# Kernel optimization log

Measured on AMD Instinct MI355X. Metric: run time of the kernel, lower is better.

## Reference

```python
import jax, jax.numpy as jnp
import numpy as np

DENSE_SIZE = 2048
BATCH = 64
MAX_SPIKES = 1024


def setup_inputs() -> dict:
    key = jax.random.key(0)
    k_w, k_ids, k_ns = jax.random.split(key, 3)
    # weights ~ N(0, 2) as in tf.random_normal_initializer(0., 2., 42)
    W = jax.random.normal(k_w, (DENSE_SIZE, DENSE_SIZE), dtype=jnp.float32) * 2.0
    spike_ids = jax.random.randint(k_ids, (BATCH, MAX_SPIKES), 0, DENSE_SIZE, dtype=jnp.int32)
    num_spikes = jax.random.randint(k_ns, (BATCH,), 0, MAX_SPIKES, dtype=jnp.int32)
    return {"spike_ids": spike_ids, "num_spikes": num_spikes, "W": W}


def reference(spike_ids, num_spikes, W):
    # Dense-weight x binary-sparse-vector matmul:
    # out[b, j] = sum_{i < num_spikes[b]} W[j, spike_ids[b, i]]
    # i.e. gather active columns of W and sum them.
    mask = (jnp.arange(MAX_SPIKES)[None, :] < num_spikes[:, None]).astype(W.dtype)  # [B, S]
    cols = jnp.take(W.T, spike_ids, axis=0)  # [B, S, D] gathered columns (rows of W.T)
    out = jnp.einsum('bs,bsd->bd', mask, cols)  # [B, D]
    return out
```

## Files before the change

kernel.cpp:

```cpp
#include <hip/hip_runtime.h>

#define DENSE 2048
#define BATCH 64
#define MAXS  1024

typedef __attribute__((ext_vector_type(8))) __bf16 bf16x8;
typedef __attribute__((ext_vector_type(4))) float f32x4;


__global__ __launch_bounds__(256) void hist_kernel(const int* __restrict__ ids,
                                                   const int* __restrict__ ns,
                                                   __bf16* __restrict__ Cbf,
                                                   float* __restrict__ out) {
    __shared__ int cnt[DENSE];
    const int b = blockIdx.x;
    const int tid = threadIdx.x;
    #pragma unroll
    for (int k = tid; k < DENSE; k += 256) cnt[k] = 0;
    __syncthreads();
    const int n = ns[b];
    const int4 v = ((const int4*)(ids + b * MAXS))[tid];
    const int base = tid * 4;
    if (base + 0 < n) atomicAdd(&cnt[v.x], 1);
    if (base + 1 < n) atomicAdd(&cnt[v.y], 1);
    if (base + 2 < n) atomicAdd(&cnt[v.z], 1);
    if (base + 3 < n) atomicAdd(&cnt[v.w], 1);
    __syncthreads();
    const int mt = b >> 4;
    const int bl = b & 15;
    #pragma unroll
    for (int k = tid; k < DENSE; k += 256) {
        const int lane = bl | (((k >> 3) & 3) << 4);
        const size_t off = (size_t)(((k >> 5) * 4 + mt) * 64 + lane) * 8 + (k & 7);
        Cbf[off] = (__bf16)(float)cnt[k];
        out[(size_t)b * DENSE + k] = 0.0f;
    }
}

__global__ __launch_bounds__(256) void spmm_kernel(const float* __restrict__ W,
                                                   const __bf16* __restrict__ Cbf,
                                                   float* __restrict__ out) {
    const int tid  = threadIdx.x;
    const int lane = tid & 63;
    const int wv   = tid >> 6;
    const int j0   = blockIdx.x * 16;
    const int ks4  = blockIdx.y;

    const int ln = lane & 15;
    const int lq = lane >> 4;

    const int step0 = ks4 * 16 + wv * 4;
    const float* wrow = W + (size_t)(j0 + ln) * DENSE;

    f32x4 w0[4], w1[4];
    #pragma unroll
    for (int s = 0; s < 4; ++s) {
        const int kbase = (step0 + s) * 32 + lq * 8;
        w0[s] = *(const f32x4*)(wrow + kbase);
        w1[s] = *(const f32x4*)(wrow + kbase + 4);
    }
    bf16x8 afr[4][4];
    #pragma unroll
    for (int s = 0; s < 4; ++s) {
        #pragma unroll
        for (int mt = 0; mt < 4; ++mt) {
            afr[s][mt] = *(const bf16x8*)(Cbf + ((size_t)((step0 + s) * 4 + mt) * 64 + lane) * 8);
        }
    }

    bf16x8 wb[4];
    #pragma unroll
    for (int s = 0; s < 4; ++s) {
        #pragma unroll
        for (int i = 0; i < 4; ++i) {
            wb[s][i]     = (__bf16)w0[s][i];
            wb[s][i + 4] = (__bf16)w1[s][i];
        }
    }

    f32x4 acc[4];
    #pragma unroll
    for (int mt = 0; mt < 4; ++mt) acc[mt] = (f32x4)0.0f;
    #pragma unroll
    for (int s = 0; s < 4; ++s) {
        #pragma unroll
        for (int mt = 0; mt < 4; ++mt) {
            acc[mt] = __builtin_amdgcn_mfma_f32_16x16x32_bf16(afr[s][mt], wb[s], acc[mt], 0, 0, 0);
        }
    }

    __shared__ float P[4][4][4][64];
    #pragma unroll
    for (int mt = 0; mt < 4; ++mt) {
        #pragma unroll
        for (int r = 0; r < 4; ++r) {
            P[wv][mt][r][lane] = acc[mt][r];
        }
    }
    __syncthreads();

    const int jloc  = tid & 15;
    const int bpart = tid >> 4;
    const int lsrc  = ((bpart >> 2) << 4) | jloc;
    const int r     = bpart & 3;
    #pragma unroll
    for (int mt = 0; mt < 4; ++mt) {
        const float v = P[0][mt][r][lsrc] + P[1][mt][r][lsrc]
                      + P[2][mt][r][lsrc] + P[3][mt][r][lsrc];
        atomicAdd(&out[(size_t)(mt * 16 + bpart) * DENSE + j0 + jloc], v);
    }
}

extern "C" void kernel_launch(void* const* d_in, const int* in_sizes, int n_in,
                              void* d_out, int out_size, void* d_ws, size_t ws_size,
                              hipStream_t stream) {
    const int*   ids = (const int*)d_in[0];
    const int*   ns  = (const int*)d_in[1];
    const float* W   = (const float*)d_in[2];
    float*  out = (float*)d_out;
    __bf16* Cbf = (__bf16*)d_ws;

    hipLaunchKernelGGL(hist_kernel, dim3(BATCH), dim3(256), 0, stream, ids, ns, Cbf, out);
    hipLaunchKernelGGL(spmm_kernel, dim3(128, 4), dim3(256), 0, stream, W, Cbf, out);
}
```

Baseline: 72.28 us.

## Prefetch W into cache during histogram, drop K-split atomics, double-buffer spmm loads

After: 78.93 us. 1.09x slower.

```diff
diff --git a/kernel.cpp b/kernel.cpp
--- a/kernel.cpp
+++ b/kernel.cpp
@@ -10,82 +10,102 @@
 
 __global__ __launch_bounds__(256) void hist_kernel(const int* __restrict__ ids,
                                                    const int* __restrict__ ns,
+                                                   const float* __restrict__ W,
                                                    __bf16* __restrict__ Cbf,
-                                                   float* __restrict__ out) {
-    __shared__ int cnt[DENSE];
-    const int b = blockIdx.x;
+                                                   float* __restrict__ guard) {
     const int tid = threadIdx.x;
-    #pragma unroll
-    for (int k = tid; k < DENSE; k += 256) cnt[k] = 0;
-    __syncthreads();
-    const int n = ns[b];
-    const int4 v = ((const int4*)(ids + b * MAXS))[tid];
-    const int base = tid * 4;
-    if (base + 0 < n) atomicAdd(&cnt[v.x], 1);
-    if (base + 1 < n) atomicAdd(&cnt[v.y], 1);
-    if (base + 2 < n) atomicAdd(&cnt[v.z], 1);
-    if (base + 3 < n) atomicAdd(&cnt[v.w], 1);
-    __syncthreads();
-    const int mt = b >> 4;
-    const int bl = b & 15;
-    #pragma unroll
-    for (int k = tid; k < DENSE; k += 256) {
-        const int lane = bl | (((k >> 3) & 3) << 4);
-        const size_t off = (size_t)(((k >> 5) * 4 + mt) * 64 + lane) * 8 + (k & 7);
-        Cbf[off] = (__bf16)(float)cnt[k];
-        out[(size_t)b * DENSE + k] = 0.0f;
+    const int bid = blockIdx.x;
+    if (bid < BATCH) {
+        __shared__ int cnt[DENSE];
+        const int b = bid;
+        #pragma unroll
+        for (int k = tid; k < DENSE; k += 256) cnt[k] = 0;
+        __syncthreads();
+        const int n = ns[b];
+        const int4 v = ((const int4*)(ids + b * MAXS))[tid];
+        const int base = tid * 4;
+        if (base + 0 < n) atomicAdd(&cnt[v.x], 1);
+        if (base + 1 < n) atomicAdd(&cnt[v.y], 1);
+        if (base + 2 < n) atomicAdd(&cnt[v.z], 1);
+        if (base + 3 < n) atomicAdd(&cnt[v.w], 1);
+        __syncthreads();
+        const int mt = b >> 4;
+        const int bl = b & 15;
+        #pragma unroll
+        for (int k = tid; k < DENSE; k += 256) {
+            const int lane = bl | (((k >> 3) & 3) << 4);
+            const size_t off = (size_t)(((k >> 5) * 4 + mt) * 64 + lane) * 8 + (k & 7);
+            Cbf[off] = (__bf16)(float)cnt[k];
+        }
+    } else {
+        const int t = (bid - BATCH) * 256 + tid;
+        float s = 0.0f;
+        for (int i = t; i < (DENSE * DENSE) / 4; i += 192 * 256) {
+            const f32x4 v = ((const f32x4*)W)[i];
+            s += v.x + v.y + v.z + v.w;
+        }
+        if (s != s) guard[0] = s;
     }
 }
 
-__global__ __launch_bounds__(256) void spmm_kernel(const float* __restrict__ W,
-                                                   const __bf16* __restrict__ Cbf,
-                                                   float* __restrict__ out) {
+__global__ __launch_bounds__(256, 1) void spmm_kernel(const float* __restrict__ W,
+                                                      const __bf16* __restrict__ Cbf,
+                                                      float* __restrict__ out) {
     const int tid  = threadIdx.x;
     const int lane = tid & 63;
     const int wv   = tid >> 6;
     const int j0   = blockIdx.x * 16;
-    const int ks4  = blockIdx.y;
 
     const int ln = lane & 15;
     const int lq = lane >> 4;
 
-    const int step0 = ks4 * 16 + wv * 4;
     const float* wrow = W + (size_t)(j0 + ln) * DENSE;
+    const int ks0 = wv * 16;
 
-    f32x4 w0[4], w1[4];
+    f32x4  w0[2][4], w1[2][4];
+    bf16x8 ca[2][4][4];
+
     #pragma unroll
     for (int s = 0; s < 4; ++s) {
-        const int kbase = (step0 + s) * 32 + lq * 8;
-        w0[s] = *(const f32x4*)(wrow + kbase);
-        w1[s] = *(const f32x4*)(wrow + kbase + 4);
-    }
-    bf16x8 afr[4][4];
-    #pragma unroll
-    for (int s = 0; s < 4; ++s) {
+        const int ks = ks0 + s;
+        const int kb = ks * 32 + lq * 8;
+        w0[0][s] = *(const f32x4*)(wrow + kb);
+        w1[0][s] = *(const f32x4*)(wrow + kb + 4);
         #pragma unroll
-        for (int mt = 0; mt < 4; ++mt) {
-            afr[s][mt] = *(const bf16x8*)(Cbf + ((size_t)((step0 + s) * 4 + mt) * 64 + lane) * 8);
-        }
-    }
-
-    bf16x8 wb[4];
-    #pragma unroll
-    for (int s = 0; s < 4; ++s) {
-        #pragma unroll
-        for (int i = 0; i < 4; ++i) {
-            wb[s][i]     = (__bf16)w0[s][i];
-            wb[s][i + 4] = (__bf16)w1[s][i];
-        }
+        for (int mt = 0; mt < 4; ++mt)
+            ca[0][s][mt] = *(const bf16x8*)(Cbf + ((size_t)(ks * 4 + mt) * 64 + lane) * 8);
     }
 
     f32x4 acc[4];
     #pragma unroll
     for (int mt = 0; mt < 4; ++mt) acc[mt] = (f32x4)0.0f;
+
     #pragma unroll
-    for (int s = 0; s < 4; ++s) {
+    for (int c = 0; c < 4; ++c) {
+        const int cur = c & 1, nxt = cur ^ 1;
+        if (c < 3) {
+            #pragma unroll
+            for (int s = 0; s < 4; ++s) {
+                const int ks = ks0 + (c + 1) * 4 + s;
+                const int kb = ks * 32 + lq * 8;
+                w0[nxt][s] = *(const f32x4*)(wrow + kb);
+                w1[nxt][s] = *(const f32x4*)(wrow + kb + 4);
+                #pragma unroll
+                for (int mt = 0; mt < 4; ++mt)
+                    ca[nxt][s][mt] = *(const bf16x8*)(Cbf + ((size_t)(ks * 4 + mt) * 64 + lane) * 8);
+            }
+        }
         #pragma unroll
-        for (int mt = 0; mt < 4; ++mt) {
-            acc[mt] = __builtin_amdgcn_mfma_f32_16x16x32_bf16(afr[s][mt], wb[s], acc[mt], 0, 0, 0);
+        for (int s = 0; s < 4; ++s) {
+            bf16x8 wb;
+            #pragma unroll
+            for (int i = 0; i < 4; ++i) {
+                wb[i]     = (__bf16)w0[cur][s][i];
+                wb[i + 4] = (__bf16)w1[cur][s][i];
+            }
+            #pragma unroll
+            for (int mt = 0; mt < 4; ++mt)
+                acc[mt] = __builtin_amdgcn_mfma_f32_16x16x32_bf16(ca[cur][s][mt], wb, acc[mt], 0, 0, 0);
         }
     }
 
@@ -99,16 +119,20 @@
     }
     __syncthreads();
 
-    const int jloc  = tid & 15;
-    const int bpart = tid >> 4;
-    const int lsrc  = ((bpart >> 2) << 4) | jloc;
-    const int r     = bpart & 3;
+    const int b   = tid >> 2;
+    const int jq  = tid & 3;
+    const int mt  = b >> 4;
+    const int m16 = b & 15;
+    const int r   = m16 & 3;
+    const int lh  = (m16 >> 2) << 4;
+    f32x4 o;
     #pragma unroll
-    for (int mt = 0; mt < 4; ++mt) {
-        const float v = P[0][mt][r][lsrc] + P[1][mt][r][lsrc]
-                      + P[2][mt][r][lsrc] + P[3][mt][r][lsrc];
-        atomicAdd(&out[(size_t)(mt * 16 + bpart) * DENSE + j0 + jloc], v);
+    for (int i = 0; i < 4; ++i) {
+        const int lsrc = lh | (jq * 4 + i);
+        o[i] = P[0][mt][r][lsrc] + P[1][mt][r][lsrc]
+             + P[2][mt][r][lsrc] + P[3][mt][r][lsrc];
     }
+    *(f32x4*)(out + (size_t)b * DENSE + j0 + jq * 4) = o;
 }
 
 extern "C" void kernel_launch(void* const* d_in, const int* in_sizes, int n_in,
@@ -119,7 +143,8 @@
     const float* W   = (const float*)d_in[2];
     float*  out = (float*)d_out;
     __bf16* Cbf = (__bf16*)d_ws;
+    float*  guard = (float*)((char*)d_ws + (1 << 20));
 
-    hipLaunchKernelGGL(hist_kernel, dim3(BATCH), dim3(256), 0, stream, ids, ns, Cbf, out);
-    hipLaunchKernelGGL(spmm_kernel, dim3(128, 4), dim3(256), 0, stream, W, Cbf, out);
+    hipLaunchKernelGGL(hist_kernel, dim3(256), dim3(256), 0, stream, ids, ns, W, Cbf, guard);
+    hipLaunchKernelGGL(spmm_kernel, dim3(128), dim3(256), 0, stream, W, Cbf, out);
 }
```
